# Performance work log

Measured on AMD Instinct MI355X. Metric: run time of the kernel, lower is better.

## Reference

```python
import jax, jax.numpy as jnp
import numpy as np

B, Q, K, C, OUT, H = 8, 1024, 1024, 16, 32, 16
WINDOW = 0.25


def _linear_params(k, fan_in, fan_out):
    s = 1.0 / np.sqrt(fan_in)
    k1, k2 = jax.random.split(k)
    W = jax.random.uniform(k1, (fan_out, fan_in), minval=-s, maxval=s)
    b = jax.random.uniform(k2, (fan_out,), minval=-s, maxval=s)
    return W, b


def setup_inputs() -> dict:
    key = jax.random.key(0)
    ks = jax.random.split(key, 12)
    channels = jax.random.randint(ks[0], (B, K), 0, C).astype(jnp.float32)
    pos = jax.random.uniform(ks[1], (B, K, 1))
    keys_in = jnp.concatenate([channels[..., None], pos], axis=-1)  # [B,K,2]
    queries = jax.random.uniform(ks[2], (B, Q, 1))
    values = jax.random.normal(ks[3], (B, K, C))
    W0, b0 = _linear_params(ks[4], C + 1, H)
    W1, b1 = _linear_params(ks[5], H, H)
    W2, b2 = _linear_params(ks[6], H, H)
    W3, b3 = _linear_params(ks[7], H, 1)
    Wd, bd = _linear_params(ks[8], 1, 1)
    Wr, br = _linear_params(ks[9], 2 * C, OUT)
    return dict(keys_in=keys_in, queries=queries, values=values,
                W0=W0, b0=b0, W1=W1, b1=b1, W2=W2, b2=b2, W3=W3, b3=b3,
                Wd=Wd, bd=bd, Wr=Wr, br=br)


def reference(keys_in, queries, values, W0, b0, W1, b1, W2, b2, W3, b3, Wd, bd, Wr, br):
    channels = keys_in[..., 0].astype(jnp.int32)          # [B,K]
    pos = keys_in[..., 1:]                                # [B,K,1]
    # abs pairwise diff (is_abs_dist=True): [B,Q,K,1]
    adiff = jnp.abs(pos[:, None, :, :] - queries[:, :, None, :])
    mask = (adiff < WINDOW).astype(adiff.dtype)           # [B,Q,K,1]
    oh = jax.nn.one_hot(channels, C, dtype=adiff.dtype)   # [B,K,C]
    # MLP first layer split to avoid materializing [B,Q,K,C+1] concat:
    # input = [adiff, one_hot]; W0 is (H, C+1) torch layout (out, in)
    h_pos = adiff * W0[:, 0]                              # [B,Q,K,H]
    h_oh = oh @ W0[:, 1:].T + b0                          # [B,K,H]
    h = jax.nn.relu(h_pos + h_oh[:, None])                # [B,Q,K,H]
    h = jax.nn.relu(h @ W1.T + b1)
    h = jax.nn.relu(h @ W2.T + b2)
    w = jnp.abs(h @ W3.T + b3) * mask                     # [B,Q,K,1]
    # is_sparse: multiply by abs of one-hot channels -> per-channel weights
    weight = w * oh[:, None]                              # [B,Q,K,C]
    density = weight.sum(axis=2)                          # [B,Q,C]
    wn = weight / (density[:, :, None, :] + 1e-5)
    vals = (oh * values)[:, None]                         # [B,1,K,C]
    targets = (wn * vals).sum(axis=2)                     # [B,Q,C]
    dens = jax.nn.sigmoid((density * 0.1 - 1.0) * Wd[0, 0] + bd[0])  # [B,Q,C]
    out = jnp.concatenate([targets, dens], axis=-1) @ Wr.T + br      # [B,Q,OUT]
    return out
```

## Files before the change

kernel.cpp:

```cpp
#include <hip/hip_runtime.h>
#include <math.h>

#define BB 8
#define QQ 1024
#define KK 1024
#define CC 16
#define NS 512
#define TSTRIDE (NS + 1)
#define TFLOATS (CC * TSTRIDE)

__global__ __launch_bounds__(256) void prep_kernel(
    const float* __restrict__ keys_in, const float* __restrict__ values,
    const float* __restrict__ W0, const float* __restrict__ b0,
    const float* __restrict__ W1, const float* __restrict__ b1,
    const float* __restrict__ W2, const float* __restrict__ b2,
    const float* __restrict__ W3, const float* __restrict__ b3,
    float* __restrict__ tbl, float* __restrict__ pos_b,
    float* __restrict__ val_b, int* __restrict__ offs_b)
{
  const int tid = threadIdx.x;
  const int blk = blockIdx.x;

  if (blk < BB) {
    __shared__ int cnt[CC];
    __shared__ int offs[CC + 1];
    __shared__ int cur[CC];
    if (tid < CC) cnt[tid] = 0;
    __syncthreads();
    for (int k = tid; k < KK; k += 256) {
      int c = (int)keys_in[blk * (2 * KK) + 2 * k];
      atomicAdd(&cnt[c], 1);
    }
    __syncthreads();
    if (tid == 0) {
      int s = 0;
      for (int c = 0; c < CC; ++c) { offs[c] = s; cur[c] = s; s += cnt[c]; }
      offs[CC] = s;
    }
    __syncthreads();
    for (int k = tid; k < KK; k += 256) {
      int c = (int)keys_in[blk * (2 * KK) + 2 * k];
      float p = keys_in[blk * (2 * KK) + 2 * k + 1];
      int idx = atomicAdd(&cur[c], 1);
      pos_b[blk * KK + idx] = p;
      val_b[blk * KK + idx] = values[(blk * KK + k) * CC + c];
    }
    __syncthreads();
    if (tid < CC + 1) offs_b[blk * 32 + tid] = offs[tid];
  } else {
    __shared__ float sW0p[16];
    __shared__ float sH[256];
    __shared__ float sW1[256], sb1[16], sW2[256], sb2[16], sW3[16], sb3[1];
    if (tid < 16) {
      sW0p[tid] = W0[tid * 17];
      sb1[tid]  = b1[tid];
      sb2[tid]  = b2[tid];
      sW3[tid]  = W3[tid];
    }
    if (tid == 0) sb3[0] = b3[0];
    {
      int i = tid >> 4, c = tid & 15;
      sH[c * 16 + i] = W0[i * 17 + 1 + c] + b0[i];
      sW1[tid] = W1[tid];
      sW2[tid] = W2[tid];
    }
    __syncthreads();

    const int total = CC * (NS + 1);
    const int stride = (gridDim.x - BB) * 256;
    for (int e = (blk - BB) * 256 + tid; e < total; e += stride) {
      int c = e / (NS + 1);
      int s = e - c * (NS + 1);
      float d = (float)s * (0.25f / (float)NS);
      float h0[16], h1[16];
#pragma unroll
      for (int i = 0; i < 16; ++i) {
        float v = fmaf(d, sW0p[i], sH[c * 16 + i]);
        h0[i] = v > 0.f ? v : 0.f;
      }
#pragma unroll
      for (int j = 0; j < 16; ++j) {
        float a = sb1[j];
#pragma unroll
        for (int i = 0; i < 16; ++i) a = fmaf(sW1[j * 16 + i], h0[i], a);
        h1[j] = a > 0.f ? a : 0.f;
      }
      float w = sb3[0];
#pragma unroll
      for (int j = 0; j < 16; ++j) {
        float a = sb2[j];
#pragma unroll
        for (int i = 0; i < 16; ++i) a = fmaf(sW2[j * 16 + i], h1[i], a);
        a = a > 0.f ? a : 0.f;
        w = fmaf(sW3[j], a, w);
      }
      tbl[c * TSTRIDE + s] = fabsf(w);
    }
  }
}

__global__ __launch_bounds__(256) void main_kernel(
    const float* __restrict__ queries,
    const float* __restrict__ Wd, const float* __restrict__ bd,
    const float* __restrict__ Wr, const float* __restrict__ br,
    const float* __restrict__ tbl, const float* __restrict__ pos_b,
    const float* __restrict__ val_b, const int* __restrict__ offs_b,
    float* __restrict__ out)
{
  __shared__ float4 tls4[TFLOATS / 4];
  __shared__ float pos_s[KK];
  __shared__ float val_s[KK];
  __shared__ int   offs_s[CC + 1];
  __shared__ float wr_s[32 * 33];
  __shared__ float br_s[32];
  __shared__ float ep_s[4][33];
  __shared__ float wdbd[2];
  float* tls = (float*)tls4;

  const int tid = threadIdx.x;
  const int b  = blockIdx.x >> 8;
  const int qt = blockIdx.x & 255;

  for (int i = tid; i < TFLOATS / 4; i += 256)
    tls4[i] = ((const float4*)tbl)[i];
  for (int k = tid; k < KK; k += 256) {
    pos_s[k] = pos_b[b * KK + k];
    val_s[k] = val_b[b * KK + k];
  }
  if (tid < CC + 1) offs_s[tid] = offs_b[b * 32 + tid];
  {
    int o = tid >> 5, j = tid & 31;
    wr_s[o * 33 + j] = Wr[tid];
    wr_s[(o + 8) * 33 + j]  = Wr[tid + 256];
    wr_s[(o + 16) * 33 + j] = Wr[tid + 512];
    wr_s[(o + 24) * 33 + j] = Wr[tid + 768];
  }
  if (tid < 32) br_s[tid] = br[tid];
  if (tid == 0) { wdbd[0] = Wd[0]; wdbd[1] = bd[0]; }
  __syncthreads();

  const int wave = tid >> 6;
  const int lane = tid & 63;
  const int q = qt * 4 + wave;
  const float qpos = queries[b * QQ + q];
  const int c = lane & 15;
  const int h = lane >> 4;

  const float* __restrict__ tc = tls + c * TSTRIDE;
  float den = 0.f, num = 0.f;
  const int kend = offs_s[c + 1];
#pragma unroll 4
  for (int k = offs_s[c] + h; k < kend; k += 4) {
    float p = pos_s[k];
    float v = val_s[k];
    float d = fabsf(p - qpos);
    float t = d * ((float)NS / 0.25f);
    int   i = (int)t;
    i = i < NS - 1 ? i : NS - 1;
    float f = t - (float)i;
    float t0 = tc[i];
    float t1 = tc[i + 1];
    float w  = fmaf(t1 - t0, f, t0);
    w = (d < 0.25f) ? w : 0.0f;
    den += w;
    num  = fmaf(w, v, num);
  }
  den += __shfl_xor(den, 16, 64);
  num += __shfl_xor(num, 16, 64);
  den += __shfl_xor(den, 32, 64);
  num += __shfl_xor(num, 32, 64);

  if (h == 0) {
    float tgt = num / (den + 1e-5f);
    float x   = fmaf(fmaf(den, 0.1f, -1.0f), wdbd[0], wdbd[1]);
    float dn  = 1.0f / (1.0f + expf(-x));
    ep_s[wave][c]      = tgt;
    ep_s[wave][16 + c] = dn;
  }
  __syncthreads();

  if (lane < 32) {
    const int o = lane;
    float acc = br_s[o];
#pragma unroll
    for (int j = 0; j < 32; ++j)
      acc = fmaf(ep_s[wave][j], wr_s[o * 33 + j], acc);
    out[(b * QQ + q) * 32 + o] = acc;
  }
}

extern "C" void kernel_launch(void* const* d_in, const int* in_sizes, int n_in,
                              void* d_out, int out_size, void* d_ws, size_t ws_size,
                              hipStream_t stream) {
  const float* keys_in = (const float*)d_in[0];
  const float* queries = (const float*)d_in[1];
  const float* values  = (const float*)d_in[2];
  const float* W0 = (const float*)d_in[3];
  const float* b0 = (const float*)d_in[4];
  const float* W1 = (const float*)d_in[5];
  const float* b1 = (const float*)d_in[6];
  const float* W2 = (const float*)d_in[7];
  const float* b2 = (const float*)d_in[8];
  const float* W3 = (const float*)d_in[9];
  const float* b3 = (const float*)d_in[10];
  const float* Wd = (const float*)d_in[11];
  const float* bd = (const float*)d_in[12];
  const float* Wr = (const float*)d_in[13];
  const float* br = (const float*)d_in[14];
  float* out = (float*)d_out;

  float* tbl   = (float*)d_ws;
  float* pos_b = tbl + TFLOATS;
  float* val_b = pos_b + BB * KK;
  int*   offs_b = (int*)(val_b + BB * KK);

  prep_kernel<<<BB + 128, 256, 0, stream>>>(keys_in, values, W0, b0, W1, b1,
                                            W2, b2, W3, b3, tbl, pos_b, val_b, offs_b);
  main_kernel<<<2048, 256, 0, stream>>>(queries, Wd, bd, Wr, br,
                                        tbl, pos_b, val_b, offs_b, out);
}
```

Before: 107.2 us.

## Process eight queries per wave and pack key position/value as float2

Each wave now handles eight queries instead of one, so the per-block load of the 33KB interpolation table and key arrays into shared memory is amortized over 32 queries and the grid shrinks from 2048 to 256 blocks. Key position and value are interleaved into a float2 buffer so each key is one LDS read and the staging copy uses float4. The cost is more registers per thread and fewer blocks (256 on a large GPU), which may leave compute units underoccupied. The output projection is spread across all 64 lanes.

```diff
diff --git a/kernel.cpp b/kernel.cpp
--- a/kernel.cpp
+++ b/kernel.cpp
@@ -8,6 +8,7 @@
 #define NS 512
 #define TSTRIDE (NS + 1)
 #define TFLOATS (CC * TSTRIDE)
+#define NQ 8
 
 __global__ __launch_bounds__(256) void prep_kernel(
     const float* __restrict__ keys_in, const float* __restrict__ values,
@@ -15,8 +16,8 @@
     const float* __restrict__ W1, const float* __restrict__ b1,
     const float* __restrict__ W2, const float* __restrict__ b2,
     const float* __restrict__ W3, const float* __restrict__ b3,
-    float* __restrict__ tbl, float* __restrict__ pos_b,
-    float* __restrict__ val_b, int* __restrict__ offs_b)
+    float* __restrict__ tbl, float2* __restrict__ pv_b,
+    int* __restrict__ offs_b)
 {
   const int tid = threadIdx.x;
   const int blk = blockIdx.x;
@@ -42,8 +43,7 @@
       int c = (int)keys_in[blk * (2 * KK) + 2 * k];
       float p = keys_in[blk * (2 * KK) + 2 * k + 1];
       int idx = atomicAdd(&cur[c], 1);
-      pos_b[blk * KK + idx] = p;
-      val_b[blk * KK + idx] = values[(blk * KK + k) * CC + c];
+      pv_b[blk * KK + idx] = make_float2(p, values[(blk * KK + k) * CC + c]);
     }
     __syncthreads();
     if (tid < CC + 1) offs_b[blk * 32 + tid] = offs[tid];
@@ -103,29 +103,29 @@
     const float* __restrict__ queries,
     const float* __restrict__ Wd, const float* __restrict__ bd,
     const float* __restrict__ Wr, const float* __restrict__ br,
-    const float* __restrict__ tbl, const float* __restrict__ pos_b,
-    const float* __restrict__ val_b, const int* __restrict__ offs_b,
+    const float* __restrict__ tbl, const float2* __restrict__ pv_b,
+    const int* __restrict__ offs_b,
     float* __restrict__ out)
 {
   __shared__ float4 tls4[TFLOATS / 4];
-  __shared__ float pos_s[KK];
-  __shared__ float val_s[KK];
+  __shared__ float2 pv_s[KK];
   __shared__ int   offs_s[CC + 1];
   __shared__ float wr_s[32 * 33];
   __shared__ float br_s[32];
-  __shared__ float ep_s[4][33];
+  __shared__ float ep_s[4][NQ][33];
   __shared__ float wdbd[2];
   float* tls = (float*)tls4;
 
   const int tid = threadIdx.x;
-  const int b  = blockIdx.x >> 8;
-  const int qt = blockIdx.x & 255;
+  const int b  = blockIdx.x >> 5;
+  const int qg = blockIdx.x & 31;
 
   for (int i = tid; i < TFLOATS / 4; i += 256)
     tls4[i] = ((const float4*)tbl)[i];
-  for (int k = tid; k < KK; k += 256) {
-    pos_s[k] = pos_b[b * KK + k];
-    val_s[k] = val_b[b * KK + k];
+  {
+    const float4* src = (const float4*)(pv_b + b * KK);
+    float4* dst = (float4*)pv_s;
+    for (int i = tid; i < KK / 2; i += 256) dst[i] = src[i];
   }
   if (tid < CC + 1) offs_s[tid] = offs_b[b * 32 + tid];
   {
@@ -141,51 +141,67 @@
 
   const int wave = tid >> 6;
   const int lane = tid & 63;
-  const int q = qt * 4 + wave;
-  const float qpos = queries[b * QQ + q];
+  const int q0 = qg * 32 + wave * NQ;
   const int c = lane & 15;
   const int h = lane >> 4;
 
+  float qpos[NQ];
+#pragma unroll
+  for (int j = 0; j < NQ; ++j) qpos[j] = queries[b * QQ + q0 + j];
+
   const float* __restrict__ tc = tls + c * TSTRIDE;
-  float den = 0.f, num = 0.f;
+  float den[NQ], num[NQ];
+#pragma unroll
+  for (int j = 0; j < NQ; ++j) { den[j] = 0.f; num[j] = 0.f; }
+
   const int kend = offs_s[c + 1];
-#pragma unroll 4
   for (int k = offs_s[c] + h; k < kend; k += 4) {
-    float p = pos_s[k];
-    float v = val_s[k];
-    float d = fabsf(p - qpos);
-    float t = d * ((float)NS / 0.25f);
-    int   i = (int)t;
-    i = i < NS - 1 ? i : NS - 1;
-    float f = t - (float)i;
-    float t0 = tc[i];
-    float t1 = tc[i + 1];
-    float w  = fmaf(t1 - t0, f, t0);
-    w = (d < 0.25f) ? w : 0.0f;
-    den += w;
-    num  = fmaf(w, v, num);
-  }
-  den += __shfl_xor(den, 16, 64);
-  num += __shfl_xor(num, 16, 64);
-  den += __shfl_xor(den, 32, 64);
-  num += __shfl_xor(num, 32, 64);
+    float2 pv = pv_s[k];
+    const float p = pv.x, v = pv.y;
+#pragma unroll
+    for (int j = 0; j < NQ; ++j) {
+      float d = fabsf(p - qpos[j]);
+      float t = d * ((float)NS / 0.25f);
+      int   i = (int)t;
+      i = i < NS - 1 ? i : NS - 1;
+      float f = t - (float)i;
+      float t0 = tc[i];
+      float t1 = tc[i + 1];
+      float w  = fmaf(t1 - t0, f, t0);
+      w = (d < 0.25f) ? w : 0.0f;
+      den[j] += w;
+      num[j] = fmaf(w, v, num[j]);
+    }
+  }
+#pragma unroll
+  for (int j = 0; j < NQ; ++j) {
+    den[j] += __shfl_xor(den[j], 16, 64);
+    num[j] += __shfl_xor(num[j], 16, 64);
+    den[j] += __shfl_xor(den[j], 32, 64);
+    num[j] += __shfl_xor(num[j], 32, 64);
+  }
 
   if (h == 0) {
-    float tgt = num / (den + 1e-5f);
-    float x   = fmaf(fmaf(den, 0.1f, -1.0f), wdbd[0], wdbd[1]);
-    float dn  = 1.0f / (1.0f + expf(-x));
-    ep_s[wave][c]      = tgt;
-    ep_s[wave][16 + c] = dn;
+#pragma unroll
+    for (int j = 0; j < NQ; ++j) {
+      float tgt = num[j] / (den[j] + 1e-5f);
+      float x   = fmaf(fmaf(den[j], 0.1f, -1.0f), wdbd[0], wdbd[1]);
+      float dn  = 1.0f / (1.0f + expf(-x));
+      ep_s[wave][j][c]      = tgt;
+      ep_s[wave][j][16 + c] = dn;
+    }
   }
   __syncthreads();
 
-  if (lane < 32) {
-    const int o = lane;
+  const int o = lane & 31;
+#pragma unroll
+  for (int jj = 0; jj < NQ / 2; ++jj) {
+    const int j = (lane >> 5) + 2 * jj;
     float acc = br_s[o];
 #pragma unroll
-    for (int j = 0; j < 32; ++j)
-      acc = fmaf(ep_s[wave][j], wr_s[o * 33 + j], acc);
-    out[(b * QQ + q) * 32 + o] = acc;
+    for (int t = 0; t < 32; ++t)
+      acc = fmaf(ep_s[wave][j][t], wr_s[o * 33 + t], acc);
+    out[(b * QQ + q0 + j) * 32 + o] = acc;
   }
 }
 
@@ -209,13 +225,12 @@
   const float* br = (const float*)d_in[14];
   float* out = (float*)d_out;
 
-  float* tbl   = (float*)d_ws;
-  float* pos_b = tbl + TFLOATS;
-  float* val_b = pos_b + BB * KK;
-  int*   offs_b = (int*)(val_b + BB * KK);
+  float*  tbl   = (float*)d_ws;
+  float2* pv_b  = (float2*)(tbl + TFLOATS);
+  int*    offs_b = (int*)(pv_b + BB * KK);
 
   prep_kernel<<<BB + 128, 256, 0, stream>>>(keys_in, values, W0, b0, W1, b1,
-                                            W2, b2, W3, b3, tbl, pos_b, val_b, offs_b);
-  main_kernel<<<2048, 256, 0, stream>>>(queries, Wd, bd, Wr, br,
-                                        tbl, pos_b, val_b, offs_b, out);
+                                            W2, b2, W3, b3, tbl, pv_b, offs_b);
+  main_kernel<<<256, 256, 0, stream>>>(queries, Wd, bd, Wr, br,
+                                       tbl, pv_b, offs_b, out);
 }
```

Measured after the change: 99.54 us. -7.1%, faster.
